# Performance work log

Hardware: AMD Instinct MI355X
Metric: run time of the kernel (lower is better)

Reference implementation:

```python
import jax, jax.numpy as jnp
import numpy as np

NUM_NODES = 100000
DIM_E = 64
NEG_SLOPE = 0.01  # F.leaky_relu default


def setup_inputs() -> dict:
    key = jax.random.key(0)
    ks = jax.random.split(key, 8)
    edge_index = jax.random.randint(ks[0], (2, 1000000), 0, NUM_NODES, dtype=jnp.int64)
    # xavier_normal for id_embedding: std = sqrt(2/(fan_in+fan_out))
    std_emb = float(np.sqrt(2.0 / (NUM_NODES + DIM_E)))
    id_embedding = jax.random.normal(ks[1], (NUM_NODES, DIM_E), dtype=jnp.float32) * std_emb
    std_w = float(np.sqrt(2.0 / (DIM_E + DIM_E)))  # glorot for GCN lin weight [out, in]
    W1 = jax.random.normal(ks[2], (DIM_E, DIM_E), dtype=jnp.float32) * std_w
    W2 = jax.random.normal(ks[3], (DIM_E, DIM_E), dtype=jnp.float32) * std_w
    W3 = jax.random.normal(ks[4], (DIM_E, DIM_E), dtype=jnp.float32) * std_w
    b1 = jnp.zeros((DIM_E,), dtype=jnp.float32)
    b2 = jnp.zeros((DIM_E,), dtype=jnp.float32)
    b3 = jnp.zeros((DIM_E,), dtype=jnp.float32)
    return {"edge_index": edge_index, "id_embedding": id_embedding,
            "W1": W1, "b1": b1, "W2": W2, "b2": b2, "W3": W3, "b3": b3}


def _build_graph(edge_index, n):
    # symmetrize (as done in RealGCN.forward) then add self loops (PyG GCNConv default)
    ei = jnp.concatenate([edge_index, edge_index[::-1]], axis=1)
    loops = jnp.arange(n, dtype=ei.dtype)
    row = jnp.concatenate([ei[0], loops])  # source
    col = jnp.concatenate([ei[1], loops])  # destination
    deg = jax.ops.segment_sum(jnp.ones_like(col, dtype=jnp.float32), col, num_segments=n)
    dinv = jnp.where(deg > 0, jax.lax.rsqrt(deg), 0.0)
    norm = dinv[row] * dinv[col]  # [E_total]
    return row, col, norm


def _gcn_conv(x, row, col, norm, W, b, n):
    h = x @ W.T                                   # [N, D] linear transform
    msg = h[row] * norm[:, None]                  # gather + normalize
    out = jax.ops.segment_sum(msg, col, num_segments=n)  # scatter-add
    return out + b


def reference(edge_index, id_embedding, W1, b1, W2, b2, W3, b3):
    n = id_embedding.shape[0]
    row, col, norm = _build_graph(edge_index, n)
    # has_norm: L2-normalize rows (F.normalize, eps=1e-12)
    nrm = jnp.linalg.norm(id_embedding, axis=1, keepdims=True)
    x = id_embedding / jnp.maximum(nrm, 1e-12)
    x1 = jax.nn.leaky_relu(_gcn_conv(x, row, col, norm, W1, b1, n), NEG_SLOPE)
    x2 = jax.nn.leaky_relu(_gcn_conv(x1, row, col, norm, W2, b2, n), NEG_SLOPE)
    x3 = _gcn_conv(x1, row, col, norm, W3, b3, n)  # note: layer 3 has no activation
    return x + x1 + x2 + x3
```

## Files before the change

### kernel.cpp

```cpp
#include <hip/hip_runtime.h>
#include <math.h>

#define DIM 64
#define NEG_SLOPE 0.01f

typedef unsigned short bfraw;
typedef unsigned int uint32;

__device__ __forceinline__ bfraw f2bf(float f) {
    unsigned int u = __float_as_uint(f);
    unsigned int r = (u + 0x7FFFu + ((u >> 16) & 1u)) >> 16;
    return (bfraw)r;
}
__device__ __forceinline__ float bflo(uint32 u) { return __uint_as_float(u << 16); }
__device__ __forceinline__ float bfhi(uint32 u) { return __uint_as_float(u & 0xFFFF0000u); }

#define EPH 8192

__global__ __launch_bounds__(256) void k_bhist(const int* __restrict__ ei, int E,
                                               int* __restrict__ bpart, int shift) {
    __shared__ int hist[256];
    int t = threadIdx.x;
    hist[t] = 0;
    __syncthreads();
    int e0 = blockIdx.x * EPH;
    int e1 = e0 + EPH < E ? e0 + EPH : E;
    for (int e = e0 + t; e < e1; e += 256) {
        int u = ei[e], v = ei[E + e];
        atomicAdd(&hist[u >> shift], 1);
        atomicAdd(&hist[v >> shift], 1);
    }
    __syncthreads();
    bpart[blockIdx.x * 256 + t] = hist[t];
}

__global__ __launch_bounds__(256) void k_bscan(const int* __restrict__ bpart, int nwgh,
                                               int nbuckets,
                                               int* __restrict__ boffs, int* __restrict__ bcur,
                                               int* __restrict__ offsets, int n, int E2) {
    __shared__ int ls[256];
    int t = threadIdx.x;
    int own = 0;
    for (int g = 0; g < nwgh; g++) own += bpart[g * 256 + t];
    ls[t] = own;
    __syncthreads();
    for (int off = 1; off < 256; off <<= 1) {
        int v = (t >= off) ? ls[t - off] : 0;
        __syncthreads();
        ls[t] += v;
        __syncthreads();
    }
    int excl = ls[t] - own;
    if (t < nbuckets) { boffs[t] = excl; bcur[t * 16] = excl; }
    if (t == 0) { boffs[nbuckets] = E2; offsets[n] = E2 + n; }
}

#define EPW 2048

__global__ __launch_bounds__(256) void k_bin(const int* __restrict__ ei, int E,
                                             uint32* __restrict__ stage,
                                             int* __restrict__ bcur, int shift, int sbits) {
    __shared__ int hist[256];
    __shared__ int cur[256];
    int t = threadIdx.x;
    hist[t] = 0;
    __syncthreads();
    int e0 = blockIdx.x * EPW;
    int e1 = e0 + EPW < E ? e0 + EPW : E;
    uint32 lmask = (1u << shift) - 1u;
    for (int e = e0 + t; e < e1; e += 256) {
        int u = ei[e], v = ei[E + e];
        atomicAdd(&hist[u >> shift], 1);
        atomicAdd(&hist[v >> shift], 1);
    }
    __syncthreads();
    cur[t] = hist[t] > 0 ? atomicAdd(&bcur[t * 16], hist[t]) : 0;
    __syncthreads();
    for (int e = e0 + t; e < e1; e += 256) {
        int u = ei[e], v = ei[E + e];
        int s1 = atomicAdd(&cur[v >> shift], 1);
        stage[s1] = (((uint32)v & lmask) << sbits) | (uint32)u;
        int s2 = atomicAdd(&cur[u >> shift], 1);
        stage[s2] = (((uint32)u & lmask) << sbits) | (uint32)v;
    }
}

__global__ __launch_bounds__(256) void k_bucket(const uint32* __restrict__ stage,
                                                const int* __restrict__ boffs,
                                                int* __restrict__ offsets,
                                                int* __restrict__ adj,
                                                float* __restrict__ dinv,
                                                int n, int shift, int sbits) {
    __shared__ int deg[2048];
    __shared__ int scan[256];
    int t = threadIdx.x;
    int span  = 1 << shift;
    int node0 = blockIdx.x << shift;
    int cnt = n - node0 < span ? n - node0 : span;
    uint32 smask = (1u << sbits) - 1u;
    for (int i = t; i < cnt; i += 256) deg[i] = 0;
    __syncthreads();
    int jbeg = boffs[blockIdx.x], jend = boffs[blockIdx.x + 1];
    for (int j = jbeg + t; j < jend; j += 256)
        atomicAdd(&deg[stage[j] >> sbits], 1);
    __syncthreads();
    int per  = span >> 8;
    int base = t * per;
    int s = 0;
    for (int k = 0; k < per; k++) { int i = base + k; if (i < cnt) s += deg[i] + 1; }
    scan[t] = s;
    __syncthreads();
    for (int off = 1; off < 256; off <<= 1) {
        int v = (t >= off) ? scan[t - off] : 0;
        __syncthreads();
        scan[t] += v;
        __syncthreads();
    }
    int run = jbeg + node0 + scan[t] - s;
    for (int k = 0; k < per; k++) {
        int i = base + k;
        if (i < cnt) {
            int d = deg[i];
            offsets[node0 + i] = run;
            dinv[node0 + i] = rsqrtf(1.0f + (float)d);
            adj[run] = node0 + i;
            deg[i] = run + 1;
            run += d + 1;
        }
    }
    __syncthreads();
    for (int j = jbeg + t; j < jend; j += 256) {
        uint32 r = stage[j];
        int slot = atomicAdd(&deg[r >> sbits], 1);
        adj[slot] = (int)(r & smask);
    }
}

__global__ void k_normalize(const float* __restrict__ x, const float* __restrict__ dinv,
                            float* __restrict__ xn, bfraw* __restrict__ xnw, int n) {
    int row  = (blockIdx.x * blockDim.x + threadIdx.x) >> 6;
    int lane = threadIdx.x & 63;
    if (row >= n) return;
    float v = x[row * DIM + lane];
    float s = v * v;
    #pragma unroll
    for (int off = 32; off; off >>= 1) s += __shfl_xor(s, off);
    float scale = 1.0f / fmaxf(sqrtf(s), 1e-12f);
    float xv = v * scale;
    xn[row * DIM + lane] = xv;
    xnw[row * DIM + lane] = f2bf(xv * dinv[row]);
}

#define ACC8(p) { a0 += bflo(p.x); a1 += bfhi(p.x); a2 += bflo(p.y); a3 += bfhi(p.y); \
                  a4 += bflo(p.z); a5 += bfhi(p.z); a6 += bflo(p.w); a7 += bfhi(p.w); }

__global__ void k_gather(const int* __restrict__ adj, const int* __restrict__ offsets,
                         const float* __restrict__ dinv,
                         const bfraw* __restrict__ srcw,
                         float* __restrict__ dst, int n) {
    int w    = (blockIdx.x * blockDim.x + threadIdx.x) >> 6;
    int lane = threadIdx.x & 63;
    if (w >= n) return;
    int oct = lane >> 3;
    int ol  = lane & 7;
    int beg = offsets[w], end = offsets[w + 1];
    float dd = dinv[w];
    const uint4* rows = (const uint4*)srcw;
    float a0 = 0.f, a1 = 0.f, a2 = 0.f, a3 = 0.f;
    float a4 = 0.f, a5 = 0.f, a6 = 0.f, a7 = 0.f;
    int j = beg;
    for (; j + 32 <= end; j += 32) {
        int s0 = adj[j + oct];
        int s1 = adj[j + 8 + oct];
        int s2 = adj[j + 16 + oct];
        int s3 = adj[j + 24 + oct];
        uint4 p0 = rows[(size_t)s0 * 8 + ol];
        uint4 p1 = rows[(size_t)s1 * 8 + ol];
        uint4 p2 = rows[(size_t)s2 * 8 + ol];
        uint4 p3 = rows[(size_t)s3 * 8 + ol];
        ACC8(p0) ACC8(p1) ACC8(p2) ACC8(p3)
    }
    if (j + 16 <= end) {
        int s0 = adj[j + oct];
        int s1 = adj[j + 8 + oct];
        uint4 p0 = rows[(size_t)s0 * 8 + ol];
        uint4 p1 = rows[(size_t)s1 * 8 + ol];
        ACC8(p0) ACC8(p1)
        j += 16;
    }
    if (j + 8 <= end) {
        int s0 = adj[j + oct];
        uint4 p0 = rows[(size_t)s0 * 8 + ol];
        ACC8(p0)
        j += 8;
    }
    int rem = end - j;
    if (oct < rem) {
        int s0 = adj[j + oct];
        uint4 p0 = rows[(size_t)s0 * 8 + ol];
        ACC8(p0)
    }
    a0 += __shfl_xor(a0, 8); a0 += __shfl_xor(a0, 16); a0 += __shfl_xor(a0, 32);
    a1 += __shfl_xor(a1, 8); a1 += __shfl_xor(a1, 16); a1 += __shfl_xor(a1, 32);
    a2 += __shfl_xor(a2, 8); a2 += __shfl_xor(a2, 16); a2 += __shfl_xor(a2, 32);
    a3 += __shfl_xor(a3, 8); a3 += __shfl_xor(a3, 16); a3 += __shfl_xor(a3, 32);
    a4 += __shfl_xor(a4, 8); a4 += __shfl_xor(a4, 16); a4 += __shfl_xor(a4, 32);
    a5 += __shfl_xor(a5, 8); a5 += __shfl_xor(a5, 16); a5 += __shfl_xor(a5, 32);
    a6 += __shfl_xor(a6, 8); a6 += __shfl_xor(a6, 16); a6 += __shfl_xor(a6, 32);
    a7 += __shfl_xor(a7, 8); a7 += __shfl_xor(a7, 16); a7 += __shfl_xor(a7, 32);
    if (lane < 8) {
        float4 o1, o2;
        o1.x = dd * a0; o1.y = dd * a1; o1.z = dd * a2; o1.w = dd * a3;
        o2.x = dd * a4; o2.y = dd * a5; o2.z = dd * a6; o2.w = dd * a7;
        float4* outp = (float4*)(dst + (size_t)w * DIM);
        outp[2 * ol]     = o1;
        outp[2 * ol + 1] = o2;
    }
}

__global__ __launch_bounds__(256) void k_linear_rt(
    const float* __restrict__ in, const float* __restrict__ W,
    const float* __restrict__ b, const float* __restrict__ dinv,
    float* __restrict__ out, bfraw* __restrict__ outw, int n)
{
    __shared__ float  sIn[64][65];
    __shared__ uint32 sWp[64][32];
    int tid = threadIdx.x;
    int r0  = blockIdx.x * 64;
    #pragma unroll
    for (int i = 0; i < 8; i++) {
        int idx = tid + i * 256;
        int k = idx & 63, cp = idx >> 6;
        sWp[k][cp] = (uint32)f2bf(W[(2 * cp) * DIM + k]) |
                     ((uint32)f2bf(W[(2 * cp + 1) * DIM + k]) << 16);
    }
    int lim = (n - r0 < 64 ? n - r0 : 64) * DIM;
    for (int idx = tid; idx < lim; idx += 256)
        sIn[idx >> 6][idx & 63] = in[(size_t)r0 * DIM + idx];
    __syncthreads();

    int ri = (tid >> 4) << 2;
    int ci = (tid & 15) << 2;
    int cp = ci >> 1;
    float acc[4][4];
    #pragma unroll
    for (int j = 0; j < 4; j++) {
        float bj = b[ci + j];
        #pragma unroll
        for (int i = 0; i < 4; i++) acc[i][j] = bj;
    }
    #pragma unroll 2
    for (int k4 = 0; k4 < 16; k4++) {
        int k = k4 * 4;
        float4 A0 = *(const float4*)&sIn[ri + 0][k];
        float4 A1 = *(const float4*)&sIn[ri + 1][k];
        float4 A2 = *(const float4*)&sIn[ri + 2][k];
        float4 A3 = *(const float4*)&sIn[ri + 3][k];
        #pragma unroll
        for (int kk = 0; kk < 4; kk++) {
            uint2 uw = *(const uint2*)&sWp[k + kk][cp];
            float w0 = bflo(uw.x), w1 = bfhi(uw.x);
            float w2 = bflo(uw.y), w3 = bfhi(uw.y);
            float a0 = kk == 0 ? A0.x : kk == 1 ? A0.y : kk == 2 ? A0.z : A0.w;
            float a1 = kk == 0 ? A1.x : kk == 1 ? A1.y : kk == 2 ? A1.z : A1.w;
            float a2 = kk == 0 ? A2.x : kk == 1 ? A2.y : kk == 2 ? A2.z : A2.w;
            float a3 = kk == 0 ? A3.x : kk == 1 ? A3.y : kk == 2 ? A3.z : A3.w;
            acc[0][0] = fmaf(a0, w0, acc[0][0]); acc[0][1] = fmaf(a0, w1, acc[0][1]);
            acc[0][2] = fmaf(a0, w2, acc[0][2]); acc[0][3] = fmaf(a0, w3, acc[0][3]);
            acc[1][0] = fmaf(a1, w0, acc[1][0]); acc[1][1] = fmaf(a1, w1, acc[1][1]);
            acc[1][2] = fmaf(a1, w2, acc[1][2]); acc[1][3] = fmaf(a1, w3, acc[1][3]);
            acc[2][0] = fmaf(a2, w0, acc[2][0]); acc[2][1] = fmaf(a2, w1, acc[2][1]);
            acc[2][2] = fmaf(a2, w2, acc[2][2]); acc[2][3] = fmaf(a2, w3, acc[2][3]);
            acc[3][0] = fmaf(a3, w0, acc[3][0]); acc[3][1] = fmaf(a3, w1, acc[3][1]);
            acc[3][2] = fmaf(a3, w2, acc[3][2]); acc[3][3] = fmaf(a3, w3, acc[3][3]);
        }
    }
    #pragma unroll
    for (int i = 0; i < 4; i++) {
        int r = r0 + ri + i;
        if (r >= n) break;
        float dd = dinv[r];
        float4 o;
        o.x = acc[i][0] > 0.f ? acc[i][0] : NEG_SLOPE * acc[i][0];
        o.y = acc[i][1] > 0.f ? acc[i][1] : NEG_SLOPE * acc[i][1];
        o.z = acc[i][2] > 0.f ? acc[i][2] : NEG_SLOPE * acc[i][2];
        o.w = acc[i][3] > 0.f ? acc[i][3] : NEG_SLOPE * acc[i][3];
        *(float4*)&out[(size_t)r * DIM + ci] = o;
        ushort4 ow;
        ow.x = f2bf(o.x * dd); ow.y = f2bf(o.y * dd);
        ow.z = f2bf(o.z * dd); ow.w = f2bf(o.w * dd);
        *(ushort4*)&outw[(size_t)r * DIM + ci] = ow;
    }
}

__global__ __launch_bounds__(256) void k_final_rt(
    const float* __restrict__ agg, const float* __restrict__ xn,
    const float* __restrict__ x1,
    const float* __restrict__ W2, const float* __restrict__ b2,
    const float* __restrict__ W3, const float* __restrict__ b3,
    float* __restrict__ out, int n)
{
    __shared__ float  sIn[64][65];
    __shared__ uint32 sW2p[64][32];
    __shared__ uint32 sW3p[64][32];
    int tid = threadIdx.x;
    int r0  = blockIdx.x * 64;
    #pragma unroll
    for (int i = 0; i < 8; i++) {
        int idx = tid + i * 256;
        int k = idx & 63, cp = idx >> 6;
        sW2p[k][cp] = (uint32)f2bf(W2[(2 * cp) * DIM + k]) |
                      ((uint32)f2bf(W2[(2 * cp + 1) * DIM + k]) << 16);
        sW3p[k][cp] = (uint32)f2bf(W3[(2 * cp) * DIM + k]) |
                      ((uint32)f2bf(W3[(2 * cp + 1) * DIM + k]) << 16);
    }
    int lim = (n - r0 < 64 ? n - r0 : 64) * DIM;
    for (int idx = tid; idx < lim; idx += 256)
        sIn[idx >> 6][idx & 63] = agg[(size_t)r0 * DIM + idx];
    __syncthreads();

    int ri = (tid >> 4) << 2;
    int ci = (tid & 15) << 2;
    int cp = ci >> 1;
    float acc2[4][4], acc3[4][4];
    #pragma unroll
    for (int j = 0; j < 4; j++) {
        float bj2 = b2[ci + j], bj3 = b3[ci + j];
        #pragma unroll
        for (int i = 0; i < 4; i++) { acc2[i][j] = bj2; acc3[i][j] = bj3; }
    }
    #pragma unroll 2
    for (int k4 = 0; k4 < 16; k4++) {
        int k = k4 * 4;
        float4 A0 = *(const float4*)&sIn[ri + 0][k];
        float4 A1 = *(const float4*)&sIn[ri + 1][k];
        float4 A2 = *(const float4*)&sIn[ri + 2][k];
        float4 A3 = *(const float4*)&sIn[ri + 3][k];
        #pragma unroll
        for (int kk = 0; kk < 4; kk++) {
            uint2 u2 = *(const uint2*)&sW2p[k + kk][cp];
            uint2 u3 = *(const uint2*)&sW3p[k + kk][cp];
            float a0 = kk == 0 ? A0.x : kk == 1 ? A0.y : kk == 2 ? A0.z : A0.w;
            float a1 = kk == 0 ? A1.x : kk == 1 ? A1.y : kk == 2 ? A1.z : A1.w;
            float a2 = kk == 0 ? A2.x : kk == 1 ? A2.y : kk == 2 ? A2.z : A2.w;
            float a3 = kk == 0 ? A3.x : kk == 1 ? A3.y : kk == 2 ? A3.z : A3.w;
            float u0 = bflo(u2.x), u1 = bfhi(u2.x), u2c = bflo(u2.y), u3c = bfhi(u2.y);
            float v0 = bflo(u3.x), v1 = bfhi(u3.x), v2c = bflo(u3.y), v3c = bfhi(u3.y);
            acc2[0][0] = fmaf(a0, u0, acc2[0][0]); acc2[0][1] = fmaf(a0, u1, acc2[0][1]);
            acc2[0][2] = fmaf(a0, u2c, acc2[0][2]); acc2[0][3] = fmaf(a0, u3c, acc2[0][3]);
            acc2[1][0] = fmaf(a1, u0, acc2[1][0]); acc2[1][1] = fmaf(a1, u1, acc2[1][1]);
            acc2[1][2] = fmaf(a1, u2c, acc2[1][2]); acc2[1][3] = fmaf(a1, u3c, acc2[1][3]);
            acc2[2][0] = fmaf(a2, u0, acc2[2][0]); acc2[2][1] = fmaf(a2, u1, acc2[2][1]);
            acc2[2][2] = fmaf(a2, u2c, acc2[2][2]); acc2[2][3] = fmaf(a2, u3c, acc2[2][3]);
            acc2[3][0] = fmaf(a3, u0, acc2[3][0]); acc2[3][1] = fmaf(a3, u1, acc2[3][1]);
            acc2[3][2] = fmaf(a3, u2c, acc2[3][2]); acc2[3][3] = fmaf(a3, u3c, acc2[3][3]);
            acc3[0][0] = fmaf(a0, v0, acc3[0][0]); acc3[0][1] = fmaf(a0, v1, acc3[0][1]);
            acc3[0][2] = fmaf(a0, v2c, acc3[0][2]); acc3[0][3] = fmaf(a0, v3c, acc3[0][3]);
            acc3[1][0] = fmaf(a1, v0, acc3[1][0]); acc3[1][1] = fmaf(a1, v1, acc3[1][1]);
            acc3[1][2] = fmaf(a1, v2c, acc3[1][2]); acc3[1][3] = fmaf(a1, v3c, acc3[1][3]);
            acc3[2][0] = fmaf(a2, v0, acc3[2][0]); acc3[2][1] = fmaf(a2, v1, acc3[2][1]);
            acc3[2][2] = fmaf(a2, v2c, acc3[2][2]); acc3[2][3] = fmaf(a2, v3c, acc3[2][3]);
            acc3[3][0] = fmaf(a3, v0, acc3[3][0]); acc3[3][1] = fmaf(a3, v1, acc3[3][1]);
            acc3[3][2] = fmaf(a3, v2c, acc3[3][2]); acc3[3][3] = fmaf(a3, v3c, acc3[3][3]);
        }
    }
    #pragma unroll
    for (int i = 0; i < 4; i++) {
        int r = r0 + ri + i;
        if (r >= n) break;
        size_t base = (size_t)r * DIM + ci;
        float4 vxn = *(const float4*)&xn[base];
        float4 vx1 = *(const float4*)&x1[base];
        float4 o;
        float e0 = acc2[i][0] > 0.f ? acc2[i][0] : NEG_SLOPE * acc2[i][0];
        float e1 = acc2[i][1] > 0.f ? acc2[i][1] : NEG_SLOPE * acc2[i][1];
        float e2 = acc2[i][2] > 0.f ? acc2[i][2] : NEG_SLOPE * acc2[i][2];
        float e3 = acc2[i][3] > 0.f ? acc2[i][3] : NEG_SLOPE * acc2[i][3];
        o.x = vxn.x + vx1.x + e0 + acc3[i][0];
        o.y = vxn.y + vx1.y + e1 + acc3[i][1];
        o.z = vxn.z + vx1.z + e2 + acc3[i][2];
        o.w = vxn.w + vx1.w + e3 + acc3[i][3];
        *(float4*)&out[base] = o;
    }
}


extern "C" void kernel_launch(void* const* d_in, const int* in_sizes, int n_in,
                              void* d_out, int out_size, void* d_ws, size_t ws_size,
                              hipStream_t stream) {
    const int*   ei  = (const int*)d_in[0];
    const float* emb = (const float*)d_in[1];
    const float* W1  = (const float*)d_in[2];
    const float* b1  = (const float*)d_in[3];
    const float* W2  = (const float*)d_in[4];
    const float* b2  = (const float*)d_in[5];
    const float* W3  = (const float*)d_in[6];
    const float* b3  = (const float*)d_in[7];
    float* out = (float*)d_out;

    int E = in_sizes[0] / 2;
    int n = in_sizes[1] / DIM;
    size_t nD = (size_t)n * DIM;

    int shift = 9;
    while ((((size_t)n + ((size_t)1 << shift) - 1) >> shift) > 256) shift++;
    int nbuckets = (int)(((size_t)n + ((size_t)1 << shift) - 1) >> shift);
    int sbits = 32 - shift;

    int nwgh = (E + EPH - 1) / EPH;

    size_t np   = ((size_t)n + 1023) & ~1023ull;
    size_t adjn = (2 * (size_t)E + np + 3) & ~3ull;
    int*   bcur    = (int*)d_ws;
    int*   boffs   = bcur + 4096;
    int*   bpart   = boffs + 512;
    int*   offsets = bpart + 512 * 256;
    float* dinv    = (float*)(offsets + np);
    float* xn      = dinv + np;
    float* x1      = xn + nD;
    float* agg     = x1 + nD;
    int*   adj     = (int*)(agg + nD);
    bfraw* xnw     = (bfraw*)(adj + adjn);
    bfraw* x1w     = xnw + nD;
    uint32* stage  = (uint32*)agg;

    const int B = 256;

    k_bhist <<<nwgh, B, 0, stream>>>(ei, E, bpart, shift);
    k_bscan <<<1, B, 0, stream>>>(bpart, nwgh, nbuckets, boffs, bcur, offsets, n, 2 * E);
    k_bin   <<<(E + EPW - 1) / EPW, B, 0, stream>>>(ei, E, stage, bcur, shift, sbits);
    k_bucket<<<nbuckets, B, 0, stream>>>(stage, boffs, offsets, adj, dinv, n, shift, sbits);

    k_normalize<<<(n + 3) / 4, B, 0, stream>>>(emb, dinv, xn, xnw, n);

    k_gather   <<<(n + 3) / 4, B, 0, stream>>>(adj, offsets, dinv, xnw, agg, n);
    k_linear_rt<<<(n + 63) / 64, B, 0, stream>>>(agg, W1, b1, dinv, x1, x1w, n);

    k_gather   <<<(n + 3) / 4, B, 0, stream>>>(adj, offsets, dinv, x1w, agg, n);
    k_final_rt <<<(n + 63) / 64, B, 0, stream>>>(agg, xn, x1, W2, b2, W3, b3, out, n);
}
```

Measured before the change: 244.4 us.

## Drop histogram and scan passes using fixed-capacity edge buckets

Removes the separate bucket-histogram and scan kernels. Each bucket instead gets a fixed capacity (about 1.25x the average edge count plus slack), and its cursor starts at b*capS. The adjacency array is padded per bucket, so each node needs an explicit end offset, which the gather kernels now read. This saves one full read of the edge list and two kernel launches, and edges per binning block are doubled. In exchange, a heavily skewed degree distribution could overflow a bucket's capacity with no check, and the padded layout uses more memory.

```diff
diff --git a/kernel.cpp b/kernel.cpp
--- a/kernel.cpp
+++ b/kernel.cpp
@@ -15,47 +15,12 @@
 __device__ __forceinline__ float bflo(uint32 u) { return __uint_as_float(u << 16); }
 __device__ __forceinline__ float bfhi(uint32 u) { return __uint_as_float(u & 0xFFFF0000u); }
 
-#define EPH 8192
-
-__global__ __launch_bounds__(256) void k_bhist(const int* __restrict__ ei, int E,
-                                               int* __restrict__ bpart, int shift) {
-    __shared__ int hist[256];
-    int t = threadIdx.x;
-    hist[t] = 0;
-    __syncthreads();
-    int e0 = blockIdx.x * EPH;
-    int e1 = e0 + EPH < E ? e0 + EPH : E;
-    for (int e = e0 + t; e < e1; e += 256) {
-        int u = ei[e], v = ei[E + e];
-        atomicAdd(&hist[u >> shift], 1);
-        atomicAdd(&hist[v >> shift], 1);
-    }
-    __syncthreads();
-    bpart[blockIdx.x * 256 + t] = hist[t];
-}
-
-__global__ __launch_bounds__(256) void k_bscan(const int* __restrict__ bpart, int nwgh,
-                                               int nbuckets,
-                                               int* __restrict__ boffs, int* __restrict__ bcur,
-                                               int* __restrict__ offsets, int n, int E2) {
-    __shared__ int ls[256];
-    int t = threadIdx.x;
-    int own = 0;
-    for (int g = 0; g < nwgh; g++) own += bpart[g * 256 + t];
-    ls[t] = own;
-    __syncthreads();
-    for (int off = 1; off < 256; off <<= 1) {
-        int v = (t >= off) ? ls[t - off] : 0;
-        __syncthreads();
-        ls[t] += v;
-        __syncthreads();
-    }
-    int excl = ls[t] - own;
-    if (t < nbuckets) { boffs[t] = excl; bcur[t * 16] = excl; }
-    if (t == 0) { boffs[nbuckets] = E2; offsets[n] = E2 + n; }
-}
-
-#define EPW 2048
+__global__ void k_initcur(int* __restrict__ bcur, int nbuckets, int capS) {
+    int b = blockIdx.x * blockDim.x + threadIdx.x;
+    if (b < nbuckets) bcur[b * 16] = b * capS;
+}
+
+#define EPW 4096
 
 __global__ __launch_bounds__(256) void k_bin(const int* __restrict__ ei, int E,
                                              uint32* __restrict__ stage,
@@ -86,11 +51,13 @@
 }
 
 __global__ __launch_bounds__(256) void k_bucket(const uint32* __restrict__ stage,
-                                                const int* __restrict__ boffs,
+                                                const int* __restrict__ bcur,
                                                 int* __restrict__ offsets,
+                                                int* __restrict__ oend,
                                                 int* __restrict__ adj,
                                                 float* __restrict__ dinv,
-                                                int n, int shift, int sbits) {
+                                                int n, int shift, int sbits,
+                                                int capS, int capA) {
     __shared__ int deg[2048];
     __shared__ int scan[256];
     int t = threadIdx.x;
@@ -100,7 +67,8 @@
     uint32 smask = (1u << sbits) - 1u;
     for (int i = t; i < cnt; i += 256) deg[i] = 0;
     __syncthreads();
-    int jbeg = boffs[blockIdx.x], jend = boffs[blockIdx.x + 1];
+    int jbeg = blockIdx.x * capS;
+    int jend = bcur[blockIdx.x * 16];
     for (int j = jbeg + t; j < jend; j += 256)
         atomicAdd(&deg[stage[j] >> sbits], 1);
     __syncthreads();
@@ -116,12 +84,13 @@
         scan[t] += v;
         __syncthreads();
     }
-    int run = jbeg + node0 + scan[t] - s;
+    int run = blockIdx.x * capA + scan[t] - s;
     for (int k = 0; k < per; k++) {
         int i = base + k;
         if (i < cnt) {
             int d = deg[i];
             offsets[node0 + i] = run;
+            oend[node0 + i]    = run + 1 + d;
             dinv[node0 + i] = rsqrtf(1.0f + (float)d);
             adj[run] = node0 + i;
             deg[i] = run + 1;
@@ -155,6 +124,7 @@
                   a4 += bflo(p.z); a5 += bfhi(p.z); a6 += bflo(p.w); a7 += bfhi(p.w); }
 
 __global__ void k_gather(const int* __restrict__ adj, const int* __restrict__ offsets,
+                         const int* __restrict__ oend,
                          const float* __restrict__ dinv,
                          const bfraw* __restrict__ srcw,
                          float* __restrict__ dst, int n) {
@@ -163,7 +133,7 @@
     if (w >= n) return;
     int oct = lane >> 3;
     int ol  = lane & 7;
-    int beg = offsets[w], end = offsets[w + 1];
+    int beg = offsets[w], end = oend[w];
     float dd = dinv[w];
     const uint4* rows = (const uint4*)srcw;
     float a0 = 0.f, a1 = 0.f, a2 = 0.f, a3 = 0.f;
@@ -406,16 +376,18 @@
     while ((((size_t)n + ((size_t)1 << shift) - 1) >> shift) > 256) shift++;
     int nbuckets = (int)(((size_t)n + ((size_t)1 << shift) - 1) >> shift);
     int sbits = 32 - shift;
-
-    int nwgh = (E + EPH - 1) / EPH;
+    int span  = 1 << shift;
+
+    int capS = (int)(2 * (size_t)E / nbuckets + (2 * (size_t)E) / (4 * (size_t)nbuckets) + 2048);
+    if ((size_t)nbuckets * capS > nD) capS = (int)(nD / nbuckets);
+    int capA = capS + span;
 
     size_t np   = ((size_t)n + 1023) & ~1023ull;
-    size_t adjn = (2 * (size_t)E + np + 3) & ~3ull;
+    size_t adjn = ((size_t)nbuckets * capA + 3) & ~3ull;
     int*   bcur    = (int*)d_ws;
-    int*   boffs   = bcur + 4096;
-    int*   bpart   = boffs + 512;
-    int*   offsets = bpart + 512 * 256;
-    float* dinv    = (float*)(offsets + np);
+    int*   offsets = bcur + 4096;
+    int*   oendA   = offsets + np;
+    float* dinv    = (float*)(oendA + np);
     float* xn      = dinv + np;
     float* x1      = xn + nD;
     float* agg     = x1 + nD;
@@ -426,16 +398,16 @@
 
     const int B = 256;
 
-    k_bhist <<<nwgh, B, 0, stream>>>(ei, E, bpart, shift);
-    k_bscan <<<1, B, 0, stream>>>(bpart, nwgh, nbuckets, boffs, bcur, offsets, n, 2 * E);
-    k_bin   <<<(E + EPW - 1) / EPW, B, 0, stream>>>(ei, E, stage, bcur, shift, sbits);
-    k_bucket<<<nbuckets, B, 0, stream>>>(stage, boffs, offsets, adj, dinv, n, shift, sbits);
+    k_initcur<<<1, B, 0, stream>>>(bcur, nbuckets, capS);
+    k_bin    <<<(E + EPW - 1) / EPW, B, 0, stream>>>(ei, E, stage, bcur, shift, sbits);
+    k_bucket <<<nbuckets, B, 0, stream>>>(stage, bcur, offsets, oendA, adj, dinv,
+                                          n, shift, sbits, capS, capA);
 
     k_normalize<<<(n + 3) / 4, B, 0, stream>>>(emb, dinv, xn, xnw, n);
 
-    k_gather   <<<(n + 3) / 4, B, 0, stream>>>(adj, offsets, dinv, xnw, agg, n);
+    k_gather   <<<(n + 3) / 4, B, 0, stream>>>(adj, offsets, oendA, dinv, xnw, agg, n);
     k_linear_rt<<<(n + 63) / 64, B, 0, stream>>>(agg, W1, b1, dinv, x1, x1w, n);
 
-    k_gather   <<<(n + 3) / 4, B, 0, stream>>>(adj, offsets, dinv, x1w, agg, n);
+    k_gather   <<<(n + 3) / 4, B, 0, stream>>>(adj, offsets, oendA, dinv, x1w, agg, n);
     k_final_rt <<<(n + 63) / 64, B, 0, stream>>>(agg, xn, x1, W2, b2, W3, b3, out, n);
 }
```

Result: slower. 253.1 us (+3.6%).
